# Kernel optimization log

Hardware: AMD Instinct MI355X
Metric: run time of the kernel (lower is better)

The kernel has to match this reference:

```python
import jax, jax.numpy as jnp
import numpy as np

MAX_SEQ_LEN = 1024
EMBED_DIM = 64


def setup_inputs() -> dict:
    key = jax.random.key(0)
    k1, k2, k3 = jax.random.split(key, 3)
    B, H, L, D = 2, 16, 1024, EMBED_DIM
    q = jax.random.normal(k1, (B, H, L, D), dtype=jnp.float32)
    k = jax.random.normal(k2, (B, H, L, D), dtype=jnp.float32)
    pos_emb = jax.random.normal(k3, (2 * MAX_SEQ_LEN - 1, D), dtype=jnp.float32)
    return {"q": q, "k": k, "pos_emb": pos_emb}


def reference(q, k, pos_emb):
    q_len = q.shape[2]
    k_len = k.shape[2]
    # relative distance index matrix, shifted and clamped into table range
    idx = jnp.arange(q_len)[:, None] - jnp.arange(k_len)[None, :] + (MAX_SEQ_LEN - 1)
    idx = jnp.clip(idx, 0, 2 * MAX_SEQ_LEN - 2)
    rel_emb = pos_emb[idx]  # [q_len, k_len, D]  (the O(Q*K*D) gather)
    # per-query batched contraction over head dim D
    bias = jnp.einsum('bhqd,qkd->bhqk', q, rel_emb)
    return bias / jnp.sqrt(jnp.asarray(EMBED_DIM, dtype=q.dtype))
```

## Files before the change

kernel.cpp:

```cpp
#include <hip/hip_runtime.h>
#include <hip/hip_bf16.h>
#include <stdint.h>


#define LSEQ 1024
#define DDIM 64

typedef __attribute__((ext_vector_type(8))) short bf16x8;
typedef __attribute__((ext_vector_type(16))) float f32x16;

__device__ __forceinline__ unsigned short f2b(float f) {
  union { float f; unsigned u; } c; c.f = f;
  unsigned u = c.u;
  u += 0x7fffu + ((u >> 16) & 1u);
  return (unsigned short)(u >> 16);
}

__global__ __launch_bounds__(256) void cvt_kernel(
    const float4* __restrict__ q4, const float4* __restrict__ p4,
    ushort4* __restrict__ qb, ushort4* __restrict__ pb) {
  int i = blockIdx.x * 256 + threadIdx.x;
  if (i < 524288) {
    float4 v = q4[i];
    ushort4 o;
    o.x = f2b(v.x * 0.125f); o.y = f2b(v.y * 0.125f);
    o.z = f2b(v.z * 0.125f); o.w = f2b(v.w * 0.125f);
    qb[i] = o;
  } else {
    int j = i - 524288;
    if (j < 32752) {
      float4 v = p4[j];
      ushort4 o;
      o.x = f2b(v.x); o.y = f2b(v.y); o.z = f2b(v.z); o.w = f2b(v.w);
      pb[j] = o;
    }
  }
}

__global__ __launch_bounds__(256) void rpe_kernel(
    const short* __restrict__ Qb, const short* __restrict__ Pb,
    float* __restrict__ out) {
  __shared__ short lds[4][2][2048];
  const int bid  = (int)blockIdx.x;
  const int q    = ((bid & 7) << 7) + (bid >> 3);
  const int tid  = (int)threadIdx.x;
  const int lane = tid & 63;
  const int wave = tid >> 6;
  const int l31  = lane & 31;
  const int hi   = lane >> 5;
  const int nbase = wave << 8;

  const int lane_off = ((lane >> 3) << 7) + ((((lane & 7) ^ (lane >> 3))) << 4);
  const char* Pc = (const char*)Pb;

  auto STAGE = [&](int tt, int buf) {
    const int lo = q + 992 - nbase - (tt << 5);
    const char* src = Pc + ((size_t)lo << 7) + lane_off;
#pragma unroll
    for (int j = 0; j < 4; ++j)
      __builtin_amdgcn_global_load_lds(
          (const __attribute__((address_space(1))) void*)(src + (j << 10)),
          (__attribute__((address_space(3))) void*)&lds[wave][buf][j << 9],
          16, 0, 0);
  };

  STAGE(0, 0);

  bf16x8 a[4];
  const short* qp = Qb + ((l31 << 10) + q) * DDIM + (hi << 3);
#pragma unroll
  for (int s = 0; s < 4; ++s)
    a[s] = *(const bf16x8*)(qp + 16 * s);

  STAGE(1, 1);

  const int rr = 31 - l31;
  const int rx = rr & 7;

  f32x16 accA, accB;
#pragma unroll
  for (int t = 0; t < 8; ++t) {
    if (t == 0 || t == 1 || t == 3 || t == 5)
      asm volatile("s_waitcnt vmcnt(4)" ::: "memory");
    else if (t == 7)
      asm volatile("s_waitcnt vmcnt(0)" ::: "memory");
    else
      asm volatile("s_waitcnt vmcnt(36)" ::: "memory");

    f32x16& acc = (t & 1) ? accB : accA;
#pragma unroll
    for (int r = 0; r < 16; ++r) acc[r] = 0.0f;

    const short* base = &lds[wave][t & 1][rr << 6];
#pragma unroll
    for (int s = 0; s < 4; ++s) {
      bf16x8 bfr = *(const bf16x8*)(base + (((hi + 2 * s) ^ rx) << 3));
      acc = __builtin_amdgcn_mfma_f32_32x32x16_bf16(a[s], bfr, acc, 0, 0, 0);
    }

    if (t & 1) {
      float* ob = out + ((size_t)hi << 22) + (q << 10) + nbase + ((t - 1) << 5) + l31;
#pragma unroll
      for (int r = 0; r < 16; ++r) {
        const int m = (r & 3) + 8 * (r >> 2);
        ob[(size_t)m << 20]      = accA[r];
        ob[((size_t)m << 20) + 32] = accB[r];
      }
    }

    if (t < 6) STAGE(t + 2, t & 1);
  }
}

extern "C" void kernel_launch(void* const* d_in, const int* in_sizes, int n_in,
                              void* d_out, int out_size, void* d_ws, size_t ws_size,
                              hipStream_t stream) {
  const float* qin = (const float*)d_in[0];
  const float* pin = (const float*)d_in[2];

  short* qb = (short*)d_ws;
  short* pb = (short*)d_ws + 2097152;

  cvt_kernel<<<2176, 256, 0, stream>>>((const float4*)qin, (const float4*)pin,
                                       (ushort4*)qb, (ushort4*)pb);
  rpe_kernel<<<1024, 256, 0, stream>>>(qb, pb, (float*)d_out);
}
```

Measured before the change: 33.86 us.

## Fuse Q fp32-to-bf16 conversion into RPE kernel and use nontemporal output stores

Removes the separate Q conversion pass: the main kernel now loads fp32 Q directly, scales it and converts it to bf16 in registers. Only the positional table is pre-converted, by a much smaller kernel. The next-tile LDS staging is issued before the output stores, the waitcnt thresholds are adjusted to match, and the output stores become nontemporal to avoid polluting cache. This trades an extra global round trip of Q for a larger per-block fp32 load and more tightly tuned vmcnt accounting.

```diff
diff --git a/kernel.cpp b/kernel.cpp
--- a/kernel.cpp
+++ b/kernel.cpp
@@ -16,29 +16,19 @@
   return (unsigned short)(u >> 16);
 }
 
-__global__ __launch_bounds__(256) void cvt_kernel(
-    const float4* __restrict__ q4, const float4* __restrict__ p4,
-    ushort4* __restrict__ qb, ushort4* __restrict__ pb) {
-  int i = blockIdx.x * 256 + threadIdx.x;
-  if (i < 524288) {
-    float4 v = q4[i];
+__global__ __launch_bounds__(256) void cvt_p_kernel(
+    const float4* __restrict__ p4, ushort4* __restrict__ pb) {
+  int j = blockIdx.x * 256 + threadIdx.x;
+  if (j < 32752) {
+    float4 v = p4[j];
     ushort4 o;
-    o.x = f2b(v.x * 0.125f); o.y = f2b(v.y * 0.125f);
-    o.z = f2b(v.z * 0.125f); o.w = f2b(v.w * 0.125f);
-    qb[i] = o;
-  } else {
-    int j = i - 524288;
-    if (j < 32752) {
-      float4 v = p4[j];
-      ushort4 o;
-      o.x = f2b(v.x); o.y = f2b(v.y); o.z = f2b(v.z); o.w = f2b(v.w);
-      pb[j] = o;
-    }
+    o.x = f2b(v.x); o.y = f2b(v.y); o.z = f2b(v.z); o.w = f2b(v.w);
+    pb[j] = o;
   }
 }
 
 __global__ __launch_bounds__(256) void rpe_kernel(
-    const short* __restrict__ Qb, const short* __restrict__ Pb,
+    const float* __restrict__ Qf, const short* __restrict__ Pb,
     float* __restrict__ out) {
   __shared__ short lds[4][2][2048];
   const int bid  = (int)blockIdx.x;
@@ -67,10 +57,20 @@
   STAGE(0, 0);
 
   bf16x8 a[4];
-  const short* qp = Qb + ((l31 << 10) + q) * DDIM + (hi << 3);
+  {
+    const float* qp = Qf + ((size_t)((l31 << 10) + q)) * DDIM + (hi << 3);
 #pragma unroll
-  for (int s = 0; s < 4; ++s)
-    a[s] = *(const bf16x8*)(qp + 16 * s);
+    for (int s = 0; s < 4; ++s) {
+      float4 u = *(const float4*)(qp + 16 * s);
+      float4 v = *(const float4*)(qp + 16 * s + 4);
+      bf16x8 t;
+      t[0] = (short)f2b(u.x * 0.125f); t[1] = (short)f2b(u.y * 0.125f);
+      t[2] = (short)f2b(u.z * 0.125f); t[3] = (short)f2b(u.w * 0.125f);
+      t[4] = (short)f2b(v.x * 0.125f); t[5] = (short)f2b(v.y * 0.125f);
+      t[6] = (short)f2b(v.z * 0.125f); t[7] = (short)f2b(v.w * 0.125f);
+      a[s] = t;
+    }
+  }
 
   STAGE(1, 1);
 
@@ -80,10 +80,10 @@
   f32x16 accA, accB;
 #pragma unroll
   for (int t = 0; t < 8; ++t) {
-    if (t == 0 || t == 1 || t == 3 || t == 5)
+    if (t == 0 || t == 1)
       asm volatile("s_waitcnt vmcnt(4)" ::: "memory");
     else if (t == 7)
-      asm volatile("s_waitcnt vmcnt(0)" ::: "memory");
+      asm volatile("s_waitcnt vmcnt(32)" ::: "memory");
     else
       asm volatile("s_waitcnt vmcnt(36)" ::: "memory");
 
@@ -98,17 +98,17 @@
       acc = __builtin_amdgcn_mfma_f32_32x32x16_bf16(a[s], bfr, acc, 0, 0, 0);
     }
 
+    if (t < 6) STAGE(t + 2, t & 1);
+
     if (t & 1) {
       float* ob = out + ((size_t)hi << 22) + (q << 10) + nbase + ((t - 1) << 5) + l31;
 #pragma unroll
       for (int r = 0; r < 16; ++r) {
         const int m = (r & 3) + 8 * (r >> 2);
-        ob[(size_t)m << 20]      = accA[r];
-        ob[((size_t)m << 20) + 32] = accB[r];
+        __builtin_nontemporal_store(accA[r], ob + ((size_t)m << 20));
+        __builtin_nontemporal_store(accB[r], ob + ((size_t)m << 20) + 32);
       }
     }
-
-    if (t < 6) STAGE(t + 2, t & 1);
   }
 }
 
@@ -118,10 +118,8 @@
   const float* qin = (const float*)d_in[0];
   const float* pin = (const float*)d_in[2];
 
-  short* qb = (short*)d_ws;
-  short* pb = (short*)d_ws + 2097152;
+  short* pb = (short*)d_ws;
 
-  cvt_kernel<<<2176, 256, 0, stream>>>((const float4*)qin, (const float4*)pin,
-                                       (ushort4*)qb, (ushort4*)pb);
-  rpe_kernel<<<1024, 256, 0, stream>>>(qb, pb, (float*)d_out);
+  cvt_p_kernel<<<128, 256, 0, stream>>>((const float4*)pin, (ushort4*)pb);
+  rpe_kernel<<<1024, 256, 0, stream>>>(qin, pb, (float*)d_out);
 }
```

New measurement: 37.49 us. 1.11x slower.
